# Performance work log

Measured on AMD Instinct MI355X. Metric: run time of the kernel, lower is better.

## Reference

```python
import jax, jax.numpy as jnp
import numpy as np

N_ENT = 200_000
N_REL = 500
IN_DIM = 128
OUT_DIM = 128
N_TRIP = 200_000
MARGIN = 6.0
EPSILON = 2.0
REL_RANGE = (MARGIN + EPSILON) / OUT_DIM  # (margin+epsilon)/out_dim
PI = 3.141592653589793
BN_EPS = 1e-5
LRELU_SLOPE = 0.01


def _embed(table, idx, max_norm=1.0):
    # torch nn.Embedding(max_norm=1) renormalizes looked-up rows to norm <= 1
    e = table[idx]
    nrm = jnp.linalg.norm(e, axis=-1, keepdims=True)
    return e * jnp.minimum(1.0, max_norm / jnp.maximum(nrm, 1e-12))


def _bn(x, gamma, beta):
    # BatchNorm1d, training mode (batch stats, biased variance)
    mu = jnp.mean(x, axis=0, keepdims=True)
    var = jnp.var(x, axis=0, keepdims=True)
    return (x - mu) * jax.lax.rsqrt(var + BN_EPS) * gamma + beta


def _rotate(triplets, ent, rel):
    # RotatE distance, mode='head_batch' (raw table indexing as in original)
    h = ent[triplets[:, 0]]
    t = ent[triplets[:, 1]]
    r = rel[triplets[:, 2]]
    re_h, im_h = jnp.split(h, 2, axis=-1)
    re_t, im_t = jnp.split(t, 2, axis=-1)
    # phase dim must match entity half-dim (in_dim//2)
    phase = (r / (REL_RANGE / PI))[:, : IN_DIM // 2]
    re_r, im_r = jnp.cos(phase), jnp.sin(phase)
    re_s = re_r * re_t + im_r * im_t - re_h
    im_s = re_r * im_t - im_r * re_t - im_h
    return jnp.sqrt(re_s * re_s + im_s * im_s).sum(-1)  # [n]


def setup_inputs() -> dict:
    key = jax.random.key(0)
    ks = jax.random.split(key, 8)
    t0 = jax.random.randint(ks[0], (N_TRIP,), 0, N_ENT)
    t1 = jax.random.randint(ks[1], (N_TRIP,), 0, N_ENT)
    t2 = jax.random.randint(ks[2], (N_TRIP,), 0, N_REL)
    triplets = jnp.stack([t0, t1, t2], axis=1)
    ent_embed = jax.random.uniform(ks[3], (N_ENT, IN_DIM), minval=-REL_RANGE, maxval=REL_RANGE, dtype=jnp.float32)
    rel_embed = jax.random.uniform(ks[4], (N_REL, IN_DIM), minval=-REL_RANGE, maxval=REL_RANGE, dtype=jnp.float32)
    # xavier_normal with gain=1.414
    W_a = jax.random.normal(ks[5], (OUT_DIM, 3 * IN_DIM), dtype=jnp.float32) * (1.414 * np.sqrt(2.0 / (3 * IN_DIM + OUT_DIM)))
    b_a = jnp.zeros((OUT_DIM,), jnp.float32)
    W_a2 = jax.random.normal(ks[6], (1, OUT_DIM), dtype=jnp.float32) * (1.414 * np.sqrt(2.0 / (OUT_DIM + 1)))
    b_a2 = jnp.zeros((1,), jnp.float32)
    gamma0 = jnp.ones((3 * IN_DIM,), jnp.float32)
    beta0 = jnp.zeros((3 * IN_DIM,), jnp.float32)
    gamma1 = jnp.ones((OUT_DIM,), jnp.float32)
    beta1 = jnp.zeros((OUT_DIM,), jnp.float32)
    return dict(triplets=triplets, ent_embed=ent_embed, rel_embed=rel_embed,
                W_a=W_a, b_a=b_a, W_a2=W_a2, b_a2=b_a2,
                gamma0=gamma0, beta0=beta0, gamma1=gamma1, beta1=beta1)


def reference(triplets, ent_embed, rel_embed, W_a, b_a, W_a2, b_a2, gamma0, beta0, gamma1, beta1):
    n = triplets.shape[0]
    e0 = _embed(ent_embed, triplets[:, 0])
    e1 = _embed(ent_embed, triplets[:, 1])
    er = _embed(rel_embed, triplets[:, 2])
    h = jnp.concatenate([jnp.concatenate([e0, e1, er], axis=1),
                         jnp.concatenate([e1, e0, -er], axis=1)], axis=0)  # [2n, 3*in_dim]
    h = _bn(h, gamma0, beta0)  # dropout in eval -> identity
    c = _bn(h @ W_a.T + b_a, gamma1, beta1)  # [2n, out_dim]
    s = c @ W_a2.T + b_a2  # [2n, 1]
    b = -jnp.where(s >= 0, s, LRELU_SLOPE * s)
    e_b = jnp.exp(b)  # [2n, 1]
    # edges[0] = cat(t0, t1): scatter-sum over edge targets (KBGAT special spmm)
    tgt = jnp.concatenate([triplets[:, 0], triplets[:, 1]])
    ebs = jax.ops.segment_sum(e_b, tgt, num_segments=N_ENT)  # [N, 1]
    temp1 = e_b * c  # [2n, out_dim]
    hs = jax.ops.segment_sum(temp1, tgt, num_segments=N_ENT)  # [N, out_dim]
    ebs = jnp.where(ebs == 0, 1e-12, ebs)
    h_ent = hs / ebs  # [N, out_dim]
    # per-relation mean of forward-edge messages minus backward-edge messages
    ridx = triplets[:, 2]
    cnt = jnp.maximum(jax.ops.segment_sum(jnp.ones((n,), temp1.dtype), ridx, num_segments=N_REL), 1.0)[:, None]
    h_rel = (jax.ops.segment_sum(temp1[:n], ridx, num_segments=N_REL)
             - jax.ops.segment_sum(temp1[n:], ridx, num_segments=N_REL)) / cnt  # [R, out_dim]
    score = MARGIN - _rotate(triplets, ent_embed, rel_embed)  # [n]
    return h_ent, h_rel, score
```

## Files before the change

kernel.cpp:

```cpp
#include <hip/hip_runtime.h>
#include <stdint.h>

#define N_TRIP 200000
#define N_ENT  200000
#define N_REL  500
#define D      128
#define MARGINF 6.0f
#define BN_EPSF 1e-5f
#define PHASE_C 50.26548245743669f
#define STAT_BLKS 256
#define BN1_BLKS  240

typedef unsigned short u16;
typedef unsigned int   u32;
typedef unsigned long long u64;
typedef __attribute__((ext_vector_type(8))) short short8;
typedef __attribute__((ext_vector_type(4))) float f32x4;
typedef __attribute__((ext_vector_type(4))) unsigned short u16x4;

__device__ inline float bfl(u32 u){ return __uint_as_float(u<<16); }
__device__ inline float bfh(u32 u){ return __uint_as_float(u&0xffff0000u); }
__device__ inline u16 f2bf(float f){
  u32 u = __float_as_uint(f);
  u32 r = (u + 0x7fffu + ((u>>16)&1u))>>16;
  return (u16)r;
}

__global__ __launch_bounds__(256) void k_hist(const int* __restrict__ trip,
    int* __restrict__ cnt0, int* __restrict__ cnt1, int* __restrict__ cntr){
  __shared__ int rc[N_REL];
  int t = threadIdx.x;
  for(int r=t; r<N_REL; r+=256) rc[r]=0;
  __syncthreads();
  #pragma unroll
  for(int k=0;k<8;k++){
    int i = blockIdx.x*2048 + t + k*256;
    if(i < N_TRIP){
      atomicAdd(&cnt0[trip[3*i]],   1);
      atomicAdd(&cnt1[trip[3*i+1]], 1);
      atomicAdd(&rc[trip[3*i+2]],   1);
    }
  }
  __syncthreads();
  for(int r=t; r<N_REL; r+=256){
    int c = rc[r];
    if(c) atomicAdd(&cntr[r], c);
  }
}

__global__ __launch_bounds__(1024) void k_scan1(const int* __restrict__ cnt0,
    const int* __restrict__ cnt1, int* __restrict__ offs, int* __restrict__ bsum){
  __shared__ int sh[1024];
  int t = threadIdx.x;
  int e = blockIdx.x*1024 + t;
  int d = (e < N_ENT) ? cnt0[e] + cnt1[e] : 0;
  sh[t] = d; __syncthreads();
  for(int st=1; st<1024; st<<=1){
    int x = (t>=st) ? sh[t-st] : 0;
    __syncthreads();
    sh[t] += x;
    __syncthreads();
  }
  if(e < N_ENT) offs[e] = sh[t] - d;
  if(t == 1023) bsum[blockIdx.x] = sh[t];
}

__global__ __launch_bounds__(512) void k_scan2(const int* __restrict__ bsum,
    int* __restrict__ boffs, const int* __restrict__ cntr,
    int* __restrict__ roffs, int* __restrict__ rcur, int nblk){
  __shared__ int sh[512];
  int t = threadIdx.x;
  int v = (t < nblk) ? bsum[t] : 0;
  sh[t] = v; __syncthreads();
  for(int st=1; st<512; st<<=1){
    int x = (t>=st) ? sh[t-st] : 0;
    __syncthreads(); sh[t] += x; __syncthreads();
  }
  if(t < nblk) boffs[t] = sh[t] - v;
  __syncthreads();
  int w = (t < N_REL) ? cntr[t] : 0;
  sh[t] = w; __syncthreads();
  for(int st=1; st<512; st<<=1){
    int x = (t>=st) ? sh[t-st] : 0;
    __syncthreads(); sh[t] += x; __syncthreads();
  }
  if(t < N_REL){ roffs[t] = sh[t]-w; rcur[t] = sh[t]-w; }
}

__global__ __launch_bounds__(1024) void k_scan3(int* __restrict__ offs,
    const int* __restrict__ boffs, int* __restrict__ cur){
  int e = blockIdx.x*1024 + threadIdx.x;
  if(e < N_ENT){
    int o = offs[e] + boffs[blockIdx.x];
    offs[e] = o;
    cur[e] = o;
  }
}

__global__ __launch_bounds__(256) void k_edges(const int* __restrict__ trip,
    int* __restrict__ cur, int* __restrict__ rcur,
    u32* __restrict__ ebuf, u64* __restrict__ pair64, u64* __restrict__ rpair){
  __shared__ int rcnt[N_REL];
  __shared__ int rbase[N_REL];
  int t = threadIdx.x;
  for(int r=t; r<N_REL; r+=256) rcnt[r]=0;
  __syncthreads();
  int i0 = blockIdx.x*2048;
  int lt0[8], lt1[8], lt2[8], lp[8];
  #pragma unroll
  for(int k=0;k<8;k++){
    int i = i0 + t + k*256;
    lt2[k] = -1;
    if(i < N_TRIP){
      int t0 = trip[3*i], t1 = trip[3*i+1], t2 = trip[3*i+2];
      lt0[k]=t0; lt1[k]=t1; lt2[k]=t2;
      lp[k] = atomicAdd(&rcnt[t2], 1);
      pair64[i] = ((u64)t2<<36) | ((u64)t1<<18) | (u64)t0;
      ebuf[atomicAdd(&cur[t0], 1)] = ((u32)t1<<10) | ((u32)t2<<1);
      ebuf[atomicAdd(&cur[t1], 1)] = ((u32)t0<<10) | ((u32)t2<<1) | 1u;
    }
  }
  __syncthreads();
  for(int r=t; r<N_REL; r+=256){
    int c = rcnt[r];
    rbase[r] = c ? atomicAdd(&rcur[r], c) : 0;
  }
  __syncthreads();
  #pragma unroll
  for(int k=0;k<8;k++){
    if(lt2[k] >= 0)
      rpair[rbase[lt2[k]] + lp[k]] =
        ((u64)lt2[k]<<36) | ((u64)lt1[k]<<18) | (u64)lt0[k];
  }
}

__global__ __launch_bounds__(256) void k_prep(const float* __restrict__ ent,
    u32* __restrict__ entnbf){
  int t = threadIdx.x, lane = t & 63;
  int l16 = lane & 15, g = lane >> 4;
  int wid = blockIdx.x*4 + (t>>6), nw = gridDim.x*4;
  for(int e8 = wid*8; e8 < N_ENT; e8 += nw*8){
    int eA = e8 + g, eB = e8 + 4 + g;
    const float* xpA = ent + (size_t)eA*D + l16*8;
    const float* xpB = ent + (size_t)eB*D + l16*8;
    float4 a0 = *(const float4*)xpA;
    float4 a1 = *(const float4*)(xpA+4);
    float4 b0 = *(const float4*)xpB;
    float4 b1 = *(const float4*)(xpB+4);
    float ssA = a0.x*a0.x + a0.y*a0.y + a0.z*a0.z + a0.w*a0.w
              + a1.x*a1.x + a1.y*a1.y + a1.z*a1.z + a1.w*a1.w;
    float ssB = b0.x*b0.x + b0.y*b0.y + b0.z*b0.z + b0.w*b0.w
              + b1.x*b1.x + b1.y*b1.y + b1.z*b1.z + b1.w*b1.w;
    #pragma unroll
    for(int o=8;o>0;o>>=1){
      ssA += __shfl_xor(ssA,o,64);
      ssB += __shfl_xor(ssB,o,64);
    }
    float nA = sqrtf(ssA), nB = sqrtf(ssB);
    float scA = nA > 1.0f ? 1.0f/nA : 1.0f;
    float scB = nB > 1.0f ? 1.0f/nB : 1.0f;
    uint4 na, nb;
    na.x = (u32)f2bf(a0.x*scA) | ((u32)f2bf(a0.y*scA)<<16);
    na.y = (u32)f2bf(a0.z*scA) | ((u32)f2bf(a0.w*scA)<<16);
    na.z = (u32)f2bf(a1.x*scA) | ((u32)f2bf(a1.y*scA)<<16);
    na.w = (u32)f2bf(a1.z*scA) | ((u32)f2bf(a1.w*scA)<<16);
    nb.x = (u32)f2bf(b0.x*scB) | ((u32)f2bf(b0.y*scB)<<16);
    nb.y = (u32)f2bf(b0.z*scB) | ((u32)f2bf(b0.w*scB)<<16);
    nb.z = (u32)f2bf(b1.x*scB) | ((u32)f2bf(b1.y*scB)<<16);
    nb.w = (u32)f2bf(b1.z*scB) | ((u32)f2bf(b1.w*scB)<<16);
    *(uint4*)(entnbf + (size_t)eA*64 + l16*4) = na;
    *(uint4*)(entnbf + (size_t)eB*64 + l16*4) = nb;
  }
}

__global__ __launch_bounds__(256) void k_stats(const u32* __restrict__ entnbf,
    const int* __restrict__ cnt0, const int* __restrict__ cnt1,
    float* __restrict__ pstat){
  __shared__ float acc[512];
  int t = threadIdx.x;
  acc[t] = 0.f; acc[t+256] = 0.f;
  __syncthreads();
  int lane = t & 63;
  int l16 = lane & 15, g = lane >> 4;
  int wid = blockIdx.x*4 + (t>>6), nw = gridDim.x*4;
  float s0[8]={0,0,0,0,0,0,0,0}, s1[8]={0,0,0,0,0,0,0,0};
  float q0[8]={0,0,0,0,0,0,0,0}, q1[8]={0,0,0,0,0,0,0,0};
  for(int e4 = wid*4; e4 < N_ENT; e4 += nw*4){
    int e = e4 + g;
    uint4 u = *(const uint4*)(entnbf + (size_t)e*64 + l16*4);
    float w0 = (float)cnt0[e], w1 = (float)cnt1[e];
    float v[8] = {bfl(u.x),bfh(u.x),bfl(u.y),bfh(u.y),
                  bfl(u.z),bfh(u.z),bfl(u.w),bfh(u.w)};
    #pragma unroll
    for(int k=0;k<8;k++){
      s0[k] += w0*v[k]; s1[k] += w1*v[k];
      q0[k] += w0*v[k]*v[k]; q1[k] += w1*v[k]*v[k];
    }
  }
  #pragma unroll
  for(int k=0;k<8;k++){
    int c = l16*8 + k;
    atomicAdd(&acc[c],     s0[k]);
    atomicAdd(&acc[128+c], s1[k]);
    atomicAdd(&acc[256+c], q0[k]);
    atomicAdd(&acc[384+c], q1[k]);
  }
  __syncthreads();
  pstat[(size_t)blockIdx.x*512 + t]       = acc[t];
  pstat[(size_t)blockIdx.x*512 + 256 + t] = acc[t+256];
}

__global__ __launch_bounds__(256) void k_redstats(const float* __restrict__ pstat,
    float* __restrict__ stats){
  int tid = blockIdx.x*256 + threadIdx.x;
  int c = tid & 511;
  int chunk = tid >> 9;
  float s = 0.f;
  #pragma unroll 4
  for(int k=0;k<STAT_BLKS/32;k++)
    s += pstat[(size_t)(chunk*(STAT_BLKS/32) + k)*512 + c];
  atomicAdd(&stats[c], s);
}

__global__ __launch_bounds__(256) void k_relstats(const float* __restrict__ rel,
    const int* __restrict__ cntr, float* __restrict__ scale_rel,
    float* __restrict__ stats, float* __restrict__ cosr, float* __restrict__ sinr){
  __shared__ float qacc[128];
  int t = threadIdx.x, lane = t & 63;
  if(t < 128) qacc[t] = 0.f;
  __syncthreads();
  int r = blockIdx.x*4 + (t>>6);
  if(r < N_REL){
    float2 x = *(const float2*)(rel + (size_t)r*D + 2*lane);
    float ss = x.x*x.x + x.y*x.y;
    #pragma unroll
    for(int o=32;o>0;o>>=1) ss += __shfl_xor(ss,o,64);
    float nrm = sqrtf(ss);
    float sc = nrm > 1.0f ? 1.0f/nrm : 1.0f;
    if(lane==0) scale_rel[r] = sc;
    float w = (float)cntr[r];
    float sx = x.x*sc, sy = x.y*sc;
    atomicAdd(&qacc[2*lane  ], w*sx*sx);
    atomicAdd(&qacc[2*lane+1], w*sy*sy);
    if(lane < 32){
      cosr[r*64 + 2*lane  ] = cosf(x.x*PHASE_C);
      sinr[r*64 + 2*lane  ] = sinf(x.x*PHASE_C);
      cosr[r*64 + 2*lane+1] = cosf(x.y*PHASE_C);
      sinr[r*64 + 2*lane+1] = sinf(x.y*PHASE_C);
    }
  }
  __syncthreads();
  if(t < 128) atomicAdd(&stats[512+t], qacc[t]);
}

__global__ __launch_bounds__(384) void k_bn0fin(const float* __restrict__ stats,
    const float* __restrict__ W_a, const float* __restrict__ b_a,
    const float* __restrict__ gamma0, const float* __restrict__ beta0,
    u16* __restrict__ Wbf, float* __restrict__ W2, float* __restrict__ bprime){
  __shared__ float a0[384], c0[384];
  int t = threadIdx.x;
  {
    int j = t & 127;
    float mu, ex2;
    if(t < 256){
      mu  = (stats[j]     + stats[128+j]) * (1.0f/(2.0f*N_TRIP));
      ex2 = (stats[256+j] + stats[384+j]) * (1.0f/(2.0f*N_TRIP));
    } else {
      mu  = 0.0f;
      ex2 = stats[512+j] * (1.0f/N_TRIP);
    }
    float var = ex2 - mu*mu;
    float a = gamma0[t]*rsqrtf(var + BN_EPSF);
    a0[t] = a;
    c0[t] = beta0[t] - mu*a;
  }
  __syncthreads();
  for(int idx=t; idx<256*128; idx+=384){
    int j = idx>>7, k = idx&127;
    int ko = ((j>>7)<<7) + k;
    Wbf[idx] = f2bf(W_a[(j&127)*384 + ko]*a0[ko]);
  }
  for(int idx=t; idx<128*128; idx+=384){
    int k = idx>>7, j = idx&127;
    W2[idx] = W_a[j*384 + 256 + k]*a0[256+k];
  }
  if(t < 128){
    float s = b_a[t];
    for(int k=0;k<384;k++) s += W_a[t*384+k]*c0[k];
    bprime[t] = s;
  }
}

__global__ __launch_bounds__(128) void k_relproj(const float* __restrict__ rel,
    const float* __restrict__ scale_rel, const float* __restrict__ W2,
    float* __restrict__ R){
  int r = blockIdx.x, j = threadIdx.x;
  __shared__ float x[128];
  x[j] = rel[(size_t)r*D + j]*scale_rel[r];
  __syncthreads();
  float s = 0.f;
  for(int k=0;k<128;k++) s += x[k]*W2[k*128+j];
  R[r*128+j] = s;
}

__global__ __launch_bounds__(256) void k_ab(const u32* __restrict__ entnbf,
    const u16* __restrict__ Wbf, u16* __restrict__ Abuf, u16* __restrict__ Bbuf){
  __shared__ u16 xlds[16*128];
  int t = threadIdx.x, lane = t & 63, q = t >> 6;
  int kgrp = (lane>>4)<<3;
  int rgrp = (lane>>4)<<2;
  int frow = lane & 15;
  short8 wf[4][4];
  #pragma unroll
  for(int jt=0;jt<4;jt++){
    #pragma unroll
    for(int kt=0;kt<4;kt++)
      wf[jt][kt] = *(const short8*)(Wbf + (size_t)(q*64 + jt*16 + frow)*D + kgrp + kt*32);
  }
  int srow = t>>4;
  int scol16 = t&15;
  char* swp = (char*)xlds + srow*256 + ((scol16<<4) ^ ((srow&7)<<4));
  const char* rdp = (const char*)xlds + frow*256;
  int rbase0 = (lane>>4)<<4;
  int fsw = (frow&7)<<4;
  for(int chunk = blockIdx.x; chunk < N_ENT/16; chunk += gridDim.x){
    uint4 pk = *(const uint4*)(entnbf + (size_t)(chunk*16 + srow)*64 + scol16*4);
    __syncthreads();
    *(uint4*)swp = pk;
    __syncthreads();
    short8 xf[4];
    #pragma unroll
    for(int kt=0;kt<4;kt++)
      xf[kt] = *(const short8*)(rdp + ((rbase0 + kt*64) ^ fsw));
    int erow = chunk*16 + frow;
    #pragma unroll
    for(int jt=0;jt<4;jt++){
      f32x4 acc = {0.f,0.f,0.f,0.f};
      #pragma unroll
      for(int kt=0;kt<4;kt++)
        acc = __builtin_amdgcn_mfma_f32_16x16x32_bf16(wf[jt][kt], xf[kt], acc, 0,0,0);
      int jbase = q*64 + jt*16 + rgrp;
      u16x4 opk;
      opk.x=f2bf(acc[0]); opk.y=f2bf(acc[1]); opk.z=f2bf(acc[2]); opk.w=f2bf(acc[3]);
      u16* dst = (jbase < 128) ? (Abuf + (size_t)erow*D + jbase)
                               : (Bbuf + (size_t)erow*D + (jbase-128));
      *(u16x4*)dst = opk;
    }
  }
}

__global__ __launch_bounds__(256) void k_bn1stats(const u64* __restrict__ pair64,
    const u16* __restrict__ A, const u16* __restrict__ B,
    const float* __restrict__ R, const float* __restrict__ bprime,
    float* __restrict__ pstat1){
  __shared__ float acc[256];
  int t = threadIdx.x;
  acc[t] = 0.f;
  __syncthreads();
  int lane = t & 63;
  int gw = blockIdx.x*4 + (t>>6), nw = gridDim.x*4;
  float bp0 = bprime[2*lane], bp1 = bprime[2*lane+1];
  float s0=0,s1=0,q0=0,q1=0;
  for(int i=4*gw; i<N_TRIP; i+=8*nw){
    {
      u64 pr = pair64[i];
      int t0 = (int)(pr & 0x3FFFF);
      int t1 = (int)((pr>>18) & 0x3FFFF);
      int t2 = (int)(pr>>36);
      u32 ua0 = *(const u32*)(A + (size_t)t0*D + 2*lane);
      u32 ua1 = *(const u32*)(A + (size_t)t1*D + 2*lane);
      u32 ub0 = *(const u32*)(B + (size_t)t0*D + 2*lane);
      u32 ub1 = *(const u32*)(B + (size_t)t1*D + 2*lane);
      float2 r = *(const float2*)(R + (size_t)t2*D + 2*lane);
      float y1x = bfl(ua0)+bfl(ub1)+r.x+bp0;
      float y1y = bfh(ua0)+bfh(ub1)+r.y+bp1;
      float y2x = bfl(ua1)+bfl(ub0)-r.x+bp0;
      float y2y = bfh(ua1)+bfh(ub0)-r.y+bp1;
      s0 += y1x+y2x; s1 += y1y+y2y;
      q0 += y1x*y1x + y2x*y2x; q1 += y1y*y1y + y2y*y2y;
    }
    int i2 = i + 4*nw;
    if(i2 < N_TRIP){
      u64 pr = pair64[i2];
      int t0 = (int)(pr & 0x3FFFF);
      int t1 = (int)((pr>>18) & 0x3FFFF);
      int t2 = (int)(pr>>36);
      u32 ua0 = *(const u32*)(A + (size_t)t0*D + 2*lane);
      u32 ua1 = *(const u32*)(A + (size_t)t1*D + 2*lane);
      u32 ub0 = *(const u32*)(B + (size_t)t0*D + 2*lane);
      u32 ub1 = *(const u32*)(B + (size_t)t1*D + 2*lane);
      float2 r = *(const float2*)(R + (size_t)t2*D + 2*lane);
      float y1x = bfl(ua0)+bfl(ub1)+r.x+bp0;
      float y1y = bfh(ua0)+bfh(ub1)+r.y+bp1;
      float y2x = bfl(ua1)+bfl(ub0)-r.x+bp0;
      float y2y = bfh(ua1)+bfh(ub0)-r.y+bp1;
      s0 += y1x+y2x; s1 += y1y+y2y;
      q0 += y1x*y1x + y2x*y2x; q1 += y1y*y1y + y2y*y2y;
    }
  }
  atomicAdd(&acc[      2*lane  ], s0);
  atomicAdd(&acc[      2*lane+1], s1);
  atomicAdd(&acc[128 + 2*lane  ], q0);
  atomicAdd(&acc[128 + 2*lane+1], q1);
  __syncthreads();
  pstat1[(size_t)blockIdx.x*256 + t] = acc[t];
}

__global__ __launch_bounds__(128) void k_bn1fin(const float* __restrict__ pstat1,
    const float* __restrict__ gamma1, const float* __restrict__ beta1,
    const float* __restrict__ W_a2, const float* __restrict__ b_a2,
    const float* __restrict__ bprime, float* __restrict__ a1c){
  __shared__ float red[128];
  int j = threadIdx.x;
  float s = 0.f, q = 0.f;
  for(int b=0;b<BN1_BLKS;b++){
    s += pstat1[(size_t)b*256 + j];
    q += pstat1[(size_t)b*256 + 128 + j];
  }
  float mu  = s*(2.0f/(float)N_TRIP);
  float var = q*(2.0f/(float)N_TRIP) - mu*mu;
  float a = gamma1[j]*rsqrtf(var + BN_EPSF);
  float cc = beta1[j] - mu*a;
  float wa1 = W_a2[j]*a;
  a1c[j]     = a;
  a1c[128+j] = cc;
  a1c[256+j] = wa1;
  red[j] = W_a2[j]*cc + wa1*bprime[j];
  __syncthreads();
  #pragma unroll
  for(int st=64; st>0; st>>=1){
    if(j < st) red[j] += red[j+st];
    __syncthreads();
  }
  if(j==0) a1c[384] = red[0] + b_a2[0];
}

__global__ __launch_bounds__(256) void k_alphabeta(const u16* __restrict__ A,
    const u16* __restrict__ B, const float* __restrict__ R,
    const float* __restrict__ a1c, float* __restrict__ alpha,
    float* __restrict__ beta, float* __restrict__ rho){
  int t = threadIdx.x, lane = t & 63;
  int l32 = lane & 31, grp = lane >> 5;
  int wid = blockIdx.x*4 + (t>>6), nw = gridDim.x*4;
  float4 wa = *(const float4*)(a1c + 256 + l32*4);
  for(int e4 = wid*4; e4 < N_ENT; e4 += nw*4){
    int eA = e4 + grp, eB = e4 + 2 + grp;
    uint2 uaA = *(const uint2*)(A + (size_t)eA*D + l32*4);
    uint2 ubA = *(const uint2*)(B + (size_t)eA*D + l32*4);
    uint2 uaB = *(const uint2*)(A + (size_t)eB*D + l32*4);
    uint2 ubB = *(const uint2*)(B + (size_t)eB*D + l32*4);
    float daA = wa.x*bfl(uaA.x) + wa.y*bfh(uaA.x) + wa.z*bfl(uaA.y) + wa.w*bfh(uaA.y);
    float dbA = wa.x*bfl(ubA.x) + wa.y*bfh(ubA.x) + wa.z*bfl(ubA.y) + wa.w*bfh(ubA.y);
    float daB = wa.x*bfl(uaB.x) + wa.y*bfh(uaB.x) + wa.z*bfl(uaB.y) + wa.w*bfh(uaB.y);
    float dbB = wa.x*bfl(ubB.x) + wa.y*bfh(ubB.x) + wa.z*bfl(ubB.y) + wa.w*bfh(ubB.y);
    #pragma unroll
    for(int o=16;o>0;o>>=1){
      daA += __shfl_xor(daA,o,64); dbA += __shfl_xor(dbA,o,64);
      daB += __shfl_xor(daB,o,64); dbB += __shfl_xor(dbB,o,64);
    }
    if(l32==0){ alpha[eA]=daA; beta[eA]=dbA; alpha[eB]=daB; beta[eB]=dbB; }
  }
  for(int r2 = wid*2 + grp; r2 < N_REL; r2 += nw*2){
    float4 rr = *(const float4*)(R + (size_t)r2*D + l32*4);
    float dr = wa.x*rr.x + wa.y*rr.y + wa.z*rr.z + wa.w*rr.w;
    #pragma unroll
    for(int o=16;o>0;o>>=1) dr += __shfl_xor(dr,o,64);
    if(l32==0) rho[r2]=dr;
  }
}

__global__ __launch_bounds__(256) void k_ent(
    const int* __restrict__ offs, const int* __restrict__ endp,
    const u32* __restrict__ ebuf,
    const u16* __restrict__ A, const u16* __restrict__ B,
    const float* __restrict__ R, const float* __restrict__ bprime,
    const float* __restrict__ a1c, const float* __restrict__ alpha,
    const float* __restrict__ beta, const float* __restrict__ rho,
    float* __restrict__ out_hent){
  int t = threadIdx.x, lane = t & 63;
  int l16 = lane & 15, g = lane >> 4;
  int wid = blockIdx.x*4 + (t>>6), nw = gridDim.x*4;
  int cb = l16*8;
  float4 bpA = *(const float4*)(bprime + cb);
  float4 bpB = *(const float4*)(bprime + cb + 4);
  float4 a1A = *(const float4*)(a1c + cb);
  float4 a1B = *(const float4*)(a1c + cb + 4);
  float4 ccA = *(const float4*)(a1c + 128 + cb);
  float4 ccB = *(const float4*)(a1c + 128 + cb + 4);
  float kap = a1c[384];
  for(int e4 = wid*4; e4 < N_ENT; e4 += nw*4){
    int e = e4 + g;
    int s = offs[e], en = endp[e];
    uint4 ua = *(const uint4*)(A + (size_t)e*D + cb);
    float ax0 = bfl(ua.x), ax1 = bfh(ua.x), ax2 = bfl(ua.y), ax3 = bfh(ua.y);
    float ax4 = bfl(ua.z), ax5 = bfh(ua.z), ax6 = bfl(ua.w), ax7 = bfh(ua.w);
    float al = alpha[e];
    float h0=0,h1=0,h2=0,h3=0,h4=0,h5=0,h6=0,h7=0, eb=0;
    int o = s;
    for(; o+1<en; o+=2){
      u32 idX = ebuf[o], idY = ebuf[o+1];
      int otX = idX>>10, r2X = (idX>>1)&511;
      int otY = idY>>10, r2Y = (idY>>1)&511;
      float sgX = (idX&1) ? -1.f : 1.f;
      float sgY = (idY&1) ? -1.f : 1.f;
      uint4 ubX = *(const uint4*)(B + (size_t)otX*D + cb);
      uint4 ubY = *(const uint4*)(B + (size_t)otY*D + cb);
      float4 rAX = *(const float4*)(R + (size_t)r2X*D + cb);
      float4 rBX = *(const float4*)(R + (size_t)r2X*D + cb + 4);
      float4 rAY = *(const float4*)(R + (size_t)r2Y*D + cb);
      float4 rBY = *(const float4*)(R + (size_t)r2Y*D + cb + 4);
      float beX = beta[otX], beY = beta[otY];
      float roX = rho[r2X],  roY = rho[r2Y];
      float svX = al + beX + sgX*roX + kap;
      float svY = al + beY + sgY*roY + kap;
      float ebX = expf(svX >= 0.f ? -svX : -0.01f*svX);
      float ebY = expf(svY >= 0.f ? -svY : -0.01f*svY);
      float y, c;
      y = ax0 + bfl(ubX.x) + sgX*rAX.x + bpA.x; c = y*a1A.x + ccA.x; h0 += ebX*c;
      y = ax1 + bfh(ubX.x) + sgX*rAX.y + bpA.y; c = y*a1A.y + ccA.y; h1 += ebX*c;
      y = ax2 + bfl(ubX.y) + sgX*rAX.z + bpA.z; c = y*a1A.z + ccA.z; h2 += ebX*c;
      y = ax3 + bfh(ubX.y) + sgX*rAX.w + bpA.w; c = y*a1A.w + ccA.w; h3 += ebX*c;
      y = ax4 + bfl(ubX.z) + sgX*rBX.x + bpB.x; c = y*a1B.x + ccB.x; h4 += ebX*c;
      y = ax5 + bfh(ubX.z) + sgX*rBX.y + bpB.y; c = y*a1B.y + ccB.y; h5 += ebX*c;
      y = ax6 + bfl(ubX.w) + sgX*rBX.z + bpB.z; c = y*a1B.z + ccB.z; h6 += ebX*c;
      y = ax7 + bfh(ubX.w) + sgX*rBX.w + bpB.w; c = y*a1B.w + ccB.w; h7 += ebX*c;
      y = ax0 + bfl(ubY.x) + sgY*rAY.x + bpA.x; c = y*a1A.x + ccA.x; h0 += ebY*c;
      y = ax1 + bfh(ubY.x) + sgY*rAY.y + bpA.y; c = y*a1A.y + ccA.y; h1 += ebY*c;
      y = ax2 + bfl(ubY.y) + sgY*rAY.z + bpA.z; c = y*a1A.z + ccA.z; h2 += ebY*c;
      y = ax3 + bfh(ubY.y) + sgY*rAY.w + bpA.w; c = y*a1A.w + ccA.w; h3 += ebY*c;
      y = ax4 + bfl(ubY.z) + sgY*rBY.x + bpB.x; c = y*a1B.x + ccB.x; h4 += ebY*c;
      y = ax5 + bfh(ubY.z) + sgY*rBY.y + bpB.y; c = y*a1B.y + ccB.y; h5 += ebY*c;
      y = ax6 + bfl(ubY.w) + sgY*rBY.z + bpB.z; c = y*a1B.z + ccB.z; h6 += ebY*c;
      y = ax7 + bfh(ubY.w) + sgY*rBY.w + bpB.w; c = y*a1B.w + ccB.w; h7 += ebY*c;
      eb += ebX + ebY;
    }
    if(o < en){
      u32 id = ebuf[o];
      int ot = id>>10, r2 = (id>>1)&511;
      float sg = (id&1) ? -1.f : 1.f;
      uint4 ub = *(const uint4*)(B + (size_t)ot*D + cb);
      float4 rA = *(const float4*)(R + (size_t)r2*D + cb);
      float4 rB = *(const float4*)(R + (size_t)r2*D + cb + 4);
      float sv = al + beta[ot] + sg*rho[r2] + kap;
      float e_b = expf(sv >= 0.f ? -sv : -0.01f*sv);
      float y, c;
      y = ax0 + bfl(ub.x) + sg*rA.x + bpA.x; c = y*a1A.x + ccA.x; h0 += e_b*c;
      y = ax1 + bfh(ub.x) + sg*rA.y + bpA.y; c = y*a1A.y + ccA.y; h1 += e_b*c;
      y = ax2 + bfl(ub.y) + sg*rA.z + bpA.z; c = y*a1A.z + ccA.z; h2 += e_b*c;
      y = ax3 + bfh(ub.y) + sg*rA.w + bpA.w; c = y*a1A.w + ccA.w; h3 += e_b*c;
      y = ax4 + bfl(ub.z) + sg*rB.x + bpB.x; c = y*a1B.x + ccB.x; h4 += e_b*c;
      y = ax5 + bfh(ub.z) + sg*rB.y + bpB.y; c = y*a1B.y + ccB.y; h5 += e_b*c;
      y = ax6 + bfl(ub.w) + sg*rB.z + bpB.z; c = y*a1B.z + ccB.z; h6 += e_b*c;
      y = ax7 + bfh(ub.w) + sg*rB.w + bpB.w; c = y*a1B.w + ccB.w; h7 += e_b*c;
      eb += e_b;
    }
    float inv = (en > s) ? 1.0f/eb : 0.0f;
    float4 o0; o0.x=h0*inv; o0.y=h1*inv; o0.z=h2*inv; o0.w=h3*inv;
    float4 o1; o1.x=h4*inv; o1.y=h5*inv; o1.z=h6*inv; o1.w=h7*inv;
    *(float4*)(out_hent + (size_t)e*D + cb)     = o0;
    *(float4*)(out_hent + (size_t)e*D + cb + 4) = o1;
  }
}

__global__ __launch_bounds__(512) void k_rel(
    const int* __restrict__ roffs, const int* __restrict__ cntr,
    const u64* __restrict__ rpair,
    const u16* __restrict__ A, const u16* __restrict__ B,
    const float* __restrict__ R, const float* __restrict__ bprime,
    const float* __restrict__ a1c, const float* __restrict__ alpha,
    const float* __restrict__ beta, const float* __restrict__ rho,
    float* __restrict__ out_hrel){
  __shared__ float red[8][128];
  int t = threadIdx.x, lane = t & 63, w = t >> 6;
  int r = blockIdx.x;
  int cnt = cntr[r], base = roffs[r];
  float2 rr = *(const float2*)(R + (size_t)r*D + 2*lane);
  float bp0 = bprime[2*lane], bp1 = bprime[2*lane+1];
  float a1x = a1c[2*lane],     a1y = a1c[2*lane+1];
  float ccx = a1c[128+2*lane], ccy = a1c[128+2*lane+1];
  float kap = a1c[384];
  float rhor = rho[r];
  float sx = 0.f, sy = 0.f;
  for(int j=w; j<cnt; j+=16){
    {
      u64 pr = rpair[base+j];
      int t0 = (int)(pr & 0x3FFFF);
      int t1 = (int)((pr>>18) & 0x3FFFF);
      float s1 = alpha[t0] + beta[t1] + rhor + kap;
      float s2 = alpha[t1] + beta[t0] - rhor + kap;
      float e1 = expf(s1 >= 0.f ? -s1 : -0.01f*s1);
      float e2 = expf(s2 >= 0.f ? -s2 : -0.01f*s2);
      u32 ua0 = *(const u32*)(A + (size_t)t0*D + 2*lane);
      u32 ua1 = *(const u32*)(A + (size_t)t1*D + 2*lane);
      u32 ub0 = *(const u32*)(B + (size_t)t0*D + 2*lane);
      u32 ub1 = *(const u32*)(B + (size_t)t1*D + 2*lane);
      float y1x = bfl(ua0)+bfl(ub1)+rr.x+bp0;
      float y1y = bfh(ua0)+bfh(ub1)+rr.y+bp1;
      float y2x = bfl(ua1)+bfl(ub0)-rr.x+bp0;
      float y2y = bfh(ua1)+bfh(ub0)-rr.y+bp1;
      float c1x = y1x*a1x+ccx, c1y = y1y*a1y+ccy;
      float c2x = y2x*a1x+ccx, c2y = y2y*a1y+ccy;
      sx += e1*c1x - e2*c2x;
      sy += e1*c1y - e2*c2y;
    }
    int j2 = j + 8;
    if(j2 < cnt){
      u64 pr = rpair[base+j2];
      int t0 = (int)(pr & 0x3FFFF);
      int t1 = (int)((pr>>18) & 0x3FFFF);
      float s1 = alpha[t0] + beta[t1] + rhor + kap;
      float s2 = alpha[t1] + beta[t0] - rhor + kap;
      float e1 = expf(s1 >= 0.f ? -s1 : -0.01f*s1);
      float e2 = expf(s2 >= 0.f ? -s2 : -0.01f*s2);
      u32 ua0 = *(const u32*)(A + (size_t)t0*D + 2*lane);
      u32 ua1 = *(const u32*)(A + (size_t)t1*D + 2*lane);
      u32 ub0 = *(const u32*)(B + (size_t)t0*D + 2*lane);
      u32 ub1 = *(const u32*)(B + (size_t)t1*D + 2*lane);
      float y1x = bfl(ua0)+bfl(ub1)+rr.x+bp0;
      float y1y = bfh(ua0)+bfh(ub1)+rr.y+bp1;
      float y2x = bfl(ua1)+bfl(ub0)-rr.x+bp0;
      float y2y = bfh(ua1)+bfh(ub0)-rr.y+bp1;
      float c1x = y1x*a1x+ccx, c1y = y1y*a1y+ccy;
      float c2x = y2x*a1x+ccx, c2y = y2y*a1y+ccy;
      sx += e1*c1x - e2*c2x;
      sy += e1*c1y - e2*c2y;
    }
  }
  float2 p; p.x = sx; p.y = sy;
  *(float2*)&red[w][2*lane] = p;
  __syncthreads();
  if(t < 128){
    float s = 0.f;
    #pragma unroll
    for(int k=0;k<8;k++) s += red[k][t];
    float cf = cnt > 0 ? (float)cnt : 1.0f;
    out_hrel[(size_t)r*D + t] = s/cf;
  }
}

__global__ __launch_bounds__(256) void k_score(const u64* __restrict__ pair64,
    const float* __restrict__ ent, const float* __restrict__ cosr,
    const float* __restrict__ sinr, float* __restrict__ score){
  int t = threadIdx.x, lane = t & 63;
  int l16 = lane & 15, g = lane >> 4;
  int wid = blockIdx.x*4 + (t>>6), nw = gridDim.x*4;
  for(int i4 = wid*4; i4 < N_TRIP; i4 += nw*4){
    int i = i4 + g;
    u64 pr = pair64[i];
    int t0 = (int)(pr & 0x3FFFF);
    int t1 = (int)((pr>>18) & 0x3FFFF);
    int t2 = (int)(pr>>36);
    float4 rh = *(const float4*)(ent + (size_t)t0*D + l16*4);
    float4 ih = *(const float4*)(ent + (size_t)t0*D + 64 + l16*4);
    float4 rt = *(const float4*)(ent + (size_t)t1*D + l16*4);
    float4 it = *(const float4*)(ent + (size_t)t1*D + 64 + l16*4);
    float4 cr = *(const float4*)(cosr + (size_t)t2*64 + l16*4);
    float4 sr = *(const float4*)(sinr + (size_t)t2*64 + l16*4);
    float rha[4] = {rh.x,rh.y,rh.z,rh.w};
    float iha[4] = {ih.x,ih.y,ih.z,ih.w};
    float rta[4] = {rt.x,rt.y,rt.z,rt.w};
    float ita[4] = {it.x,it.y,it.z,it.w};
    float cca[4] = {cr.x,cr.y,cr.z,cr.w};
    float ssa[4] = {sr.x,sr.y,sr.z,sr.w};
    float d = 0.f;
    #pragma unroll
    for(int k=0;k<4;k++){
      float res = cca[k]*rta[k] + ssa[k]*ita[k] - rha[k];
      float ims = cca[k]*ita[k] - ssa[k]*rta[k] - iha[k];
      d += sqrtf(res*res + ims*ims);
    }
    #pragma unroll
    for(int o=8;o>0;o>>=1) d += __shfl_xor(d,o,64);
    if(l16==0) score[i] = MARGINF - d;
  }
}

extern "C" void kernel_launch(void* const* d_in, const int* in_sizes, int n_in,
                              void* d_out, int out_size, void* d_ws, size_t ws_size,
                              hipStream_t stream){
  const int*   trip   = (const int*)  d_in[0];
  const float* ent    = (const float*)d_in[1];
  const float* rel    = (const float*)d_in[2];
  const float* W_a    = (const float*)d_in[3];
  const float* b_a    = (const float*)d_in[4];
  const float* W_a2   = (const float*)d_in[5];
  const float* b_a2   = (const float*)d_in[6];
  const float* gamma0 = (const float*)d_in[7];
  const float* beta0  = (const float*)d_in[8];
  const float* gamma1 = (const float*)d_in[9];
  const float* beta1  = (const float*)d_in[10];

  char* ws = (char*)d_ws;
  size_t off = 0;
  auto take = [&](size_t bytes)->void*{
    void* p = ws + off;
    off += (bytes + 255) & ~(size_t)255;
    return p;
  };
  int*   cnt0    = (int*)  take((size_t)N_ENT*4);
  int*   cnt1    = (int*)  take((size_t)N_ENT*4);
  int*   cntr    = (int*)  take((size_t)N_REL*4);
  float* stats   = (float*)take(640*4);
  size_t zero_bytes = off;
  int*   offs      = (int*)  take((size_t)N_ENT*4);
  int*   cur       = (int*)  take((size_t)N_ENT*4);
  int*   bsum      = (int*)  take(512*4);
  int*   boffs     = (int*)  take(512*4);
  int*   roffs     = (int*)  take(512*4);
  int*   rcur      = (int*)  take(512*4);
  u32*   ebuf      = (u32*)  take((size_t)2*N_TRIP*4);
  u64*   pair64    = (u64*)  take((size_t)N_TRIP*8);
  u64*   rpair     = (u64*)  take((size_t)N_TRIP*8);
  float* scale_rel = (float*)take((size_t)N_REL*4);
  u16*   Wbf       = (u16*)  take(256*128*2);
  float* W2        = (float*)take(128*128*4);
  float* bprime    = (float*)take(128*4);
  float* a1c       = (float*)take(512*4);
  float* R         = (float*)take((size_t)N_REL*D*4);
  float* cosr      = (float*)take((size_t)N_REL*64*4);
  float* sinr      = (float*)take((size_t)N_REL*64*4);
  float* alpha     = (float*)take((size_t)N_ENT*4);
  float* betab     = (float*)take((size_t)N_ENT*4);
  float* rho       = (float*)take(512*4);
  float* pstat     = (float*)take((size_t)STAT_BLKS*512*4);
  float* pstat1    = (float*)take((size_t)BN1_BLKS*256*4);
  u16*   Abuf      = (u16*)  take((size_t)N_ENT*D*2);
  u16*   Bbuf      = (u16*)  take((size_t)N_ENT*D*2);
  u32*   entnbf    = (u32*)  take((size_t)N_ENT*64*4);
  (void)ws_size; (void)n_in; (void)in_sizes; (void)out_size;

  float* out_hent  = (float*)d_out;
  float* out_hrel  = out_hent + (size_t)N_ENT*D;
  float* out_score = out_hrel + (size_t)N_REL*D;

  hipMemsetAsync(d_ws, 0, zero_bytes, stream);

  const int SCAN_BLKS = (N_ENT + 1023)/1024;
  const int EDG_BLKS  = (N_TRIP + 2047)/2048;
  k_hist     <<<EDG_BLKS, 256, 0, stream>>>(trip, cnt0, cnt1, cntr);
  k_prep     <<<2048, 256, 0, stream>>>(ent, entnbf);
  k_stats    <<<STAT_BLKS, 256, 0, stream>>>(entnbf, cnt0, cnt1, pstat);
  k_redstats <<<64, 256, 0, stream>>>(pstat, stats);
  k_scan1    <<<SCAN_BLKS, 1024, 0, stream>>>(cnt0, cnt1, offs, bsum);
  k_scan2    <<<1, 512, 0, stream>>>(bsum, boffs, cntr, roffs, rcur, SCAN_BLKS);
  k_scan3    <<<SCAN_BLKS, 1024, 0, stream>>>(offs, boffs, cur);
  k_edges    <<<EDG_BLKS, 256, 0, stream>>>(trip, cur, rcur, ebuf, pair64, rpair);
  k_relstats <<<(N_REL+3)/4, 256, 0, stream>>>(rel, cntr, scale_rel, stats, cosr, sinr);
  k_bn0fin   <<<1, 384, 0, stream>>>(stats, W_a, b_a, gamma0, beta0, Wbf, W2, bprime);
  k_relproj  <<<N_REL, 128, 0, stream>>>(rel, scale_rel, W2, R);
  k_ab       <<<2048, 256, 0, stream>>>(entnbf, Wbf, Abuf, Bbuf);
  k_bn1stats <<<BN1_BLKS, 256, 0, stream>>>(pair64, Abuf, Bbuf, R, bprime, pstat1);
  k_bn1fin   <<<1, 128, 0, stream>>>(pstat1, gamma1, beta1, W_a2, b_a2, bprime, a1c);
  k_alphabeta<<<2048, 256, 0, stream>>>(Abuf, Bbuf, R, a1c, alpha, betab, rho);
  k_ent      <<<2048, 256, 0, stream>>>(offs, cur, ebuf, Abuf, Bbuf, R,
                                        bprime, a1c, alpha, betab, rho, out_hent);
  k_rel      <<<N_REL, 512, 0, stream>>>(roffs, cntr, rpair, Abuf, Bbuf, R,
                                         bprime, a1c, alpha, betab, rho, out_hrel);
  k_score    <<<2048, 256, 0, stream>>>(pair64, ent, cosr, sinr, out_score);
}
```

Baseline: 405.5 us.

## Fold attention weight into W for alpha/beta and gather bf16 entities in score

Precomputes u = Wbf^T·wa1 in the BN1 finalize kernel so alpha/beta become dot products over the 128-dim normalized bf16 entity rows, instead of reading both projected A and B buffers. Separately, the prep kernel writes an unnormalized bf16 copy of the entity table, which the score kernel gathers in place of fp32 rows, halving gather bytes. The bf16 path is used only when the workspace is large enough. It adds a serial 128-step loop in a single-block kernel, an extra table write in prep, and lower precision in the score.

```diff
diff --git a/kernel.cpp b/kernel.cpp
--- a/kernel.cpp
+++ b/kernel.cpp
@@ -20,6 +20,7 @@
 
 __device__ inline float bfl(u32 u){ return __uint_as_float(u<<16); }
 __device__ inline float bfh(u32 u){ return __uint_as_float(u&0xffff0000u); }
+__device__ inline float bfu(u16 u){ return __uint_as_float(((u32)u)<<16); }
 __device__ inline u16 f2bf(float f){
   u32 u = __float_as_uint(f);
   u32 r = (u + 0x7fffu + ((u>>16)&1u))>>16;
@@ -135,7 +136,7 @@
 }
 
 __global__ __launch_bounds__(256) void k_prep(const float* __restrict__ ent,
-    u32* __restrict__ entnbf){
+    u32* __restrict__ entnbf, u32* entbf){
   int t = threadIdx.x, lane = t & 63;
   int l16 = lane & 15, g = lane >> 4;
   int wid = blockIdx.x*4 + (t>>6), nw = gridDim.x*4;
@@ -147,6 +148,19 @@
     float4 a1 = *(const float4*)(xpA+4);
     float4 b0 = *(const float4*)xpB;
     float4 b1 = *(const float4*)(xpB+4);
+    if(entbf){
+      uint4 pa, pb;
+      pa.x = (u32)f2bf(a0.x) | ((u32)f2bf(a0.y)<<16);
+      pa.y = (u32)f2bf(a0.z) | ((u32)f2bf(a0.w)<<16);
+      pa.z = (u32)f2bf(a1.x) | ((u32)f2bf(a1.y)<<16);
+      pa.w = (u32)f2bf(a1.z) | ((u32)f2bf(a1.w)<<16);
+      pb.x = (u32)f2bf(b0.x) | ((u32)f2bf(b0.y)<<16);
+      pb.y = (u32)f2bf(b0.z) | ((u32)f2bf(b0.w)<<16);
+      pb.z = (u32)f2bf(b1.x) | ((u32)f2bf(b1.y)<<16);
+      pb.w = (u32)f2bf(b1.z) | ((u32)f2bf(b1.w)<<16);
+      *(uint4*)(entbf + (size_t)eA*64 + l16*4) = pa;
+      *(uint4*)(entbf + (size_t)eB*64 + l16*4) = pb;
+    }
     float ssA = a0.x*a0.x + a0.y*a0.y + a0.z*a0.z + a0.w*a0.w
               + a1.x*a1.x + a1.y*a1.y + a1.z*a1.z + a1.w*a1.w;
     float ssB = b0.x*b0.x + b0.y*b0.y + b0.z*b0.z + b0.w*b0.w
@@ -409,8 +423,10 @@
 __global__ __launch_bounds__(128) void k_bn1fin(const float* __restrict__ pstat1,
     const float* __restrict__ gamma1, const float* __restrict__ beta1,
     const float* __restrict__ W_a2, const float* __restrict__ b_a2,
-    const float* __restrict__ bprime, float* __restrict__ a1c){
+    const float* __restrict__ bprime, const u16* __restrict__ Wbf,
+    float* __restrict__ a1c){
   __shared__ float red[128];
+  __shared__ float swa1[128];
   int j = threadIdx.x;
   float s = 0.f, q = 0.f;
   for(int b=0;b<BN1_BLKS;b++){
@@ -425,8 +441,17 @@
   a1c[j]     = a;
   a1c[128+j] = cc;
   a1c[256+j] = wa1;
+  swa1[j] = wa1;
   red[j] = W_a2[j]*cc + wa1*bprime[j];
   __syncthreads();
+  float uA = 0.f, uB = 0.f;
+  for(int jj=0; jj<128; jj++){
+    float w = swa1[jj];
+    uA += w*bfu(Wbf[jj*D + j]);
+    uB += w*bfu(Wbf[(128+jj)*D + j]);
+  }
+  a1c[512+j] = uA;
+  a1c[640+j] = uB;
   #pragma unroll
   for(int st=64; st>0; st>>=1){
     if(j < st) red[j] += red[j+st];
@@ -435,37 +460,46 @@
   if(j==0) a1c[384] = red[0] + b_a2[0];
 }
 
-__global__ __launch_bounds__(256) void k_alphabeta(const u16* __restrict__ A,
-    const u16* __restrict__ B, const float* __restrict__ R,
-    const float* __restrict__ a1c, float* __restrict__ alpha,
-    float* __restrict__ beta, float* __restrict__ rho){
+__global__ __launch_bounds__(256) void k_alphabeta(const u32* __restrict__ entnbf,
+    const float* __restrict__ R, const float* __restrict__ a1c,
+    float* __restrict__ alpha, float* __restrict__ beta, float* __restrict__ rho){
   int t = threadIdx.x, lane = t & 63;
-  int l32 = lane & 31, grp = lane >> 5;
+  int l16 = lane & 15, g = lane >> 4;
   int wid = blockIdx.x*4 + (t>>6), nw = gridDim.x*4;
-  float4 wa = *(const float4*)(a1c + 256 + l32*4);
+  int cb = l16*8;
+  float4 uA0 = *(const float4*)(a1c + 512 + cb);
+  float4 uA1 = *(const float4*)(a1c + 512 + cb + 4);
+  float4 uB0 = *(const float4*)(a1c + 640 + cb);
+  float4 uB1 = *(const float4*)(a1c + 640 + cb + 4);
   for(int e4 = wid*4; e4 < N_ENT; e4 += nw*4){
-    int eA = e4 + grp, eB = e4 + 2 + grp;
-    uint2 uaA = *(const uint2*)(A + (size_t)eA*D + l32*4);
-    uint2 ubA = *(const uint2*)(B + (size_t)eA*D + l32*4);
-    uint2 uaB = *(const uint2*)(A + (size_t)eB*D + l32*4);
-    uint2 ubB = *(const uint2*)(B + (size_t)eB*D + l32*4);
-    float daA = wa.x*bfl(uaA.x) + wa.y*bfh(uaA.x) + wa.z*bfl(uaA.y) + wa.w*bfh(uaA.y);
-    float dbA = wa.x*bfl(ubA.x) + wa.y*bfh(ubA.x) + wa.z*bfl(ubA.y) + wa.w*bfh(ubA.y);
-    float daB = wa.x*bfl(uaB.x) + wa.y*bfh(uaB.x) + wa.z*bfl(uaB.y) + wa.w*bfh(uaB.y);
-    float dbB = wa.x*bfl(ubB.x) + wa.y*bfh(ubB.x) + wa.z*bfl(ubB.y) + wa.w*bfh(ubB.y);
-    #pragma unroll
-    for(int o=16;o>0;o>>=1){
-      daA += __shfl_xor(daA,o,64); dbA += __shfl_xor(dbA,o,64);
-      daB += __shfl_xor(daB,o,64); dbB += __shfl_xor(dbB,o,64);
-    }
-    if(l32==0){ alpha[eA]=daA; beta[eA]=dbA; alpha[eB]=daB; beta[eB]=dbB; }
-  }
-  for(int r2 = wid*2 + grp; r2 < N_REL; r2 += nw*2){
-    float4 rr = *(const float4*)(R + (size_t)r2*D + l32*4);
-    float dr = wa.x*rr.x + wa.y*rr.y + wa.z*rr.z + wa.w*rr.w;
-    #pragma unroll
-    for(int o=16;o>0;o>>=1) dr += __shfl_xor(dr,o,64);
-    if(l32==0) rho[r2]=dr;
+    int e = e4 + g;
+    uint4 u = *(const uint4*)(entnbf + (size_t)e*64 + l16*4);
+    float v0=bfl(u.x), v1=bfh(u.x), v2=bfl(u.y), v3=bfh(u.y);
+    float v4=bfl(u.z), v5=bfh(u.z), v6=bfl(u.w), v7=bfh(u.w);
+    float da = v0*uA0.x + v1*uA0.y + v2*uA0.z + v3*uA0.w
+             + v4*uA1.x + v5*uA1.y + v6*uA1.z + v7*uA1.w;
+    float db = v0*uB0.x + v1*uB0.y + v2*uB0.z + v3*uB0.w
+             + v4*uB1.x + v5*uB1.y + v6*uB1.z + v7*uB1.w;
+    #pragma unroll
+    for(int o=8;o>0;o>>=1){
+      da += __shfl_xor(da,o,64);
+      db += __shfl_xor(db,o,64);
+    }
+    if(l16==0){ alpha[e]=da; beta[e]=db; }
+  }
+  float4 w0 = *(const float4*)(a1c + 256 + cb);
+  float4 w1 = *(const float4*)(a1c + 256 + cb + 4);
+  for(int r4 = wid*4; r4 < N_REL; r4 += nw*4){
+    int r = r4 + g;
+    if(r < N_REL){
+      float4 rA = *(const float4*)(R + (size_t)r*D + cb);
+      float4 rB = *(const float4*)(R + (size_t)r*D + cb + 4);
+      float dr = rA.x*w0.x + rA.y*w0.y + rA.z*w0.z + rA.w*w0.w
+               + rB.x*w1.x + rB.y*w1.y + rB.z*w1.z + rB.w*w1.w;
+      #pragma unroll
+      for(int o=8;o>0;o>>=1) dr += __shfl_xor(dr,o,64);
+      if(l16==0) rho[r]=dr;
+    }
   }
 }
 
@@ -638,7 +672,44 @@
   }
 }
 
-__global__ __launch_bounds__(256) void k_score(const u64* __restrict__ pair64,
+__global__ __launch_bounds__(256) void k_score_bf(const u64* __restrict__ pair64,
+    const u32* __restrict__ entbf, const float* __restrict__ cosr,
+    const float* __restrict__ sinr, float* __restrict__ score){
+  int t = threadIdx.x, lane = t & 63;
+  int l16 = lane & 15, g = lane >> 4;
+  int wid = blockIdx.x*4 + (t>>6), nw = gridDim.x*4;
+  for(int i4 = wid*4; i4 < N_TRIP; i4 += nw*4){
+    int i = i4 + g;
+    u64 pr = pair64[i];
+    int t0 = (int)(pr & 0x3FFFF);
+    int t1 = (int)((pr>>18) & 0x3FFFF);
+    int t2 = (int)(pr>>36);
+    uint2 reh = *(const uint2*)(entbf + (size_t)t0*64 + l16*2);
+    uint2 imh = *(const uint2*)(entbf + (size_t)t0*64 + 32 + l16*2);
+    uint2 ret = *(const uint2*)(entbf + (size_t)t1*64 + l16*2);
+    uint2 imt = *(const uint2*)(entbf + (size_t)t1*64 + 32 + l16*2);
+    float4 cr = *(const float4*)(cosr + (size_t)t2*64 + l16*4);
+    float4 sr = *(const float4*)(sinr + (size_t)t2*64 + l16*4);
+    float rh[4] = {bfl(reh.x),bfh(reh.x),bfl(reh.y),bfh(reh.y)};
+    float ih[4] = {bfl(imh.x),bfh(imh.x),bfl(imh.y),bfh(imh.y)};
+    float rt[4] = {bfl(ret.x),bfh(ret.x),bfl(ret.y),bfh(ret.y)};
+    float it[4] = {bfl(imt.x),bfh(imt.x),bfl(imt.y),bfh(imt.y)};
+    float cc[4] = {cr.x,cr.y,cr.z,cr.w};
+    float ss[4] = {sr.x,sr.y,sr.z,sr.w};
+    float d = 0.f;
+    #pragma unroll
+    for(int k=0;k<4;k++){
+      float res = cc[k]*rt[k] + ss[k]*it[k] - rh[k];
+      float ims = cc[k]*it[k] - ss[k]*rt[k] - ih[k];
+      d += sqrtf(res*res + ims*ims);
+    }
+    #pragma unroll
+    for(int o=8;o>0;o>>=1) d += __shfl_xor(d,o,64);
+    if(l16==0) score[i] = MARGINF - d;
+  }
+}
+
+__global__ __launch_bounds__(256) void k_score_fp(const u64* __restrict__ pair64,
     const float* __restrict__ ent, const float* __restrict__ cosr,
     const float* __restrict__ sinr, float* __restrict__ score){
   int t = threadIdx.x, lane = t & 63;
@@ -715,7 +786,7 @@
   u16*   Wbf       = (u16*)  take(256*128*2);
   float* W2        = (float*)take(128*128*4);
   float* bprime    = (float*)take(128*4);
-  float* a1c       = (float*)take(512*4);
+  float* a1c       = (float*)take(768*4);
   float* R         = (float*)take((size_t)N_REL*D*4);
   float* cosr      = (float*)take((size_t)N_REL*64*4);
   float* sinr      = (float*)take((size_t)N_REL*64*4);
@@ -727,7 +798,9 @@
   u16*   Abuf      = (u16*)  take((size_t)N_ENT*D*2);
   u16*   Bbuf      = (u16*)  take((size_t)N_ENT*D*2);
   u32*   entnbf    = (u32*)  take((size_t)N_ENT*64*4);
-  (void)ws_size; (void)n_in; (void)in_sizes; (void)out_size;
+  u32*   entbf     = (u32*)  take((size_t)N_ENT*64*4);
+  bool use_bf = (off <= ws_size);
+  (void)n_in; (void)in_sizes; (void)out_size;
 
   float* out_hent  = (float*)d_out;
   float* out_hrel  = out_hent + (size_t)N_ENT*D;
@@ -738,7 +811,7 @@
   const int SCAN_BLKS = (N_ENT + 1023)/1024;
   const int EDG_BLKS  = (N_TRIP + 2047)/2048;
   k_hist     <<<EDG_BLKS, 256, 0, stream>>>(trip, cnt0, cnt1, cntr);
-  k_prep     <<<2048, 256, 0, stream>>>(ent, entnbf);
+  k_prep     <<<2048, 256, 0, stream>>>(ent, entnbf, use_bf ? entbf : (u32*)nullptr);
   k_stats    <<<STAT_BLKS, 256, 0, stream>>>(entnbf, cnt0, cnt1, pstat);
   k_redstats <<<64, 256, 0, stream>>>(pstat, stats);
   k_scan1    <<<SCAN_BLKS, 1024, 0, stream>>>(cnt0, cnt1, offs, bsum);
@@ -750,11 +823,14 @@
   k_relproj  <<<N_REL, 128, 0, stream>>>(rel, scale_rel, W2, R);
   k_ab       <<<2048, 256, 0, stream>>>(entnbf, Wbf, Abuf, Bbuf);
   k_bn1stats <<<BN1_BLKS, 256, 0, stream>>>(pair64, Abuf, Bbuf, R, bprime, pstat1);
-  k_bn1fin   <<<1, 128, 0, stream>>>(pstat1, gamma1, beta1, W_a2, b_a2, bprime, a1c);
-  k_alphabeta<<<2048, 256, 0, stream>>>(Abuf, Bbuf, R, a1c, alpha, betab, rho);
+  k_bn1fin   <<<1, 128, 0, stream>>>(pstat1, gamma1, beta1, W_a2, b_a2, bprime, Wbf, a1c);
+  k_alphabeta<<<2048, 256, 0, stream>>>(entnbf, R, a1c, alpha, betab, rho);
   k_ent      <<<2048, 256, 0, stream>>>(offs, cur, ebuf, Abuf, Bbuf, R,
                                         bprime, a1c, alpha, betab, rho, out_hent);
   k_rel      <<<N_REL, 512, 0, stream>>>(roffs, cntr, rpair, Abuf, Bbuf, R,
                                          bprime, a1c, alpha, betab, rho, out_hrel);
-  k_score    <<<2048, 256, 0, stream>>>(pair64, ent, cosr, sinr, out_score);
-}
+  if(use_bf)
+    k_score_bf<<<2048, 256, 0, stream>>>(pair64, entbf, cosr, sinr, out_score);
+  else
+    k_score_fp<<<2048, 256, 0, stream>>>(pair64, ent, cosr, sinr, out_score);
+}
```

Measured after the change: 411.7 us. No clear change (+1.5%).
